# Kernel tuning notes

Hardware: AMD Instinct MI355X
Metric: run time of the kernel (lower is better)

The kernel has to match this reference:

```python
import jax, jax.numpy as jnp
import numpy as np

C, H, W = 3, 224, 224
P = 14  # patches per row
PS = H // P  # 16
PATCH_DIM = C * PS * PS  # 768
HIDDEN = 768


def patchify(images):
    # images: [n, c, h, w] -> [n, P*P, c*PS*PS], flatten order (c, ph, pw)
    n = images.shape[0]
    x = images.reshape(n, C, P, PS, P, PS)
    x = x.transpose(0, 2, 4, 1, 3, 5)  # [n, Pi, Pj, c, ps, ps]
    return x.reshape(n, P * P, PATCH_DIM)


def setup_inputs() -> dict:
    key = jax.random.key(0)
    k1, k2, k3 = jax.random.split(key, 3)
    images = jax.random.normal(k1, (128, C, H, W), dtype=jnp.float32)
    # nn.Linear(patch_embedding_dim, hidden_dim): weight [out, in], bias [out]
    bound = 1.0 / np.sqrt(PATCH_DIM)
    W_lin = jax.random.uniform(k2, (HIDDEN, PATCH_DIM), minval=-bound, maxval=bound, dtype=jnp.float32)
    b_lin = jax.random.uniform(k3, (HIDDEN,), minval=-bound, maxval=bound, dtype=jnp.float32)
    cls_token = jnp.ones((1, HIDDEN), dtype=jnp.float32)
    return {"images": images, "W_lin": W_lin, "b_lin": b_lin, "cls_token": cls_token}


def reference(images, W_lin, b_lin, cls_token):
    patches = patchify(images)                        # [n, 196, 768]
    hidden = jnp.einsum('npd,hd->nph', patches, W_lin) + b_lin  # [n, 196, H]
    n = images.shape[0]
    cls = jnp.broadcast_to(cls_token[None], (n, 1, HIDDEN))
    return jnp.concatenate([cls, hidden], axis=1)     # [n, 197, H]
```

## Files before the change

### kernel.cpp

```cpp
#include <hip/hip_runtime.h>
#include <cstdint>


#define PGRID 14
#define PSZ   16
#define CHN   3
#define IMGW  224
#define KDIM  768
#define NDIM  768
#define NPATCH 196
#define K32   24

typedef short bf16x8 __attribute__((ext_vector_type(8)));
typedef short short8v __attribute__((ext_vector_type(8)));
typedef float f32x4  __attribute__((ext_vector_type(4)));

__device__ __forceinline__ short bf16rne(float f) {
    uint32_t u = __builtin_bit_cast(uint32_t, f);
    u += 0x7FFFu + ((u >> 16) & 1u);
    return (short)(u >> 16);
}

__device__ __forceinline__ short8v cvt8(float4 v0, float4 v1) {
    short8v s;
    s[0] = bf16rne(v0.x); s[1] = bf16rne(v0.y); s[2] = bf16rne(v0.z); s[3] = bf16rne(v0.w);
    s[4] = bf16rne(v1.x); s[5] = bf16rne(v1.y); s[6] = bf16rne(v1.z); s[7] = bf16rne(v1.w);
    return s;
}

__global__ __launch_bounds__(256) void prep_patch(
    const float* __restrict__ img, short* __restrict__ A, int M)
{
    int t = blockIdx.x * 256 + threadIdx.x;
    if (t >= M * 96) return;
    int mlow = t & 15;
    int r    = t >> 4;
    int G    = r / 96;
    int k8   = r - G * 96;
    int m    = G * 16 + mlow;
    int k  = k8 * 8;
    int c  = k >> 8;
    int ph = (k >> 4) & 15;
    int pw = k & 15;
    int im = m / NPATCH;
    int p  = m - im * NPATCH;
    int Pi = p / PGRID;
    int Pj = p - Pi * PGRID;
    const float* src = img + (((long)(im * CHN + c) * IMGW + Pi * PSZ + ph) * IMGW + Pj * PSZ + pw);
    float4 v0 = *(const float4*)src;
    float4 v1 = *(const float4*)(src + 4);
    int k32  = k8 >> 2;
    int quad = k8 & 3;
    int lane = mlow | (quad << 4);
    *(short8v*)(A + (((long)G * K32 + k32) << 9) + lane * 8) = cvt8(v0, v1);
}

__global__ __launch_bounds__(256) void prep_small(
    const float* __restrict__ Wl, const float* __restrict__ cls,
    short* __restrict__ Wb, float* __restrict__ out, int n_img)
{
    int t = blockIdx.x * 256 + threadIdx.x;
    const int WCH = KDIM * NDIM / 8;
    if (t < WCH) {
        int nlow = t & 15;
        int r    = t >> 4;
        int G    = r / 96;
        int k8   = r - G * 96;
        int n    = G * 16 + nlow;
        float4 v0 = *(const float4*)(Wl + (long)n * KDIM + k8 * 8);
        float4 v1 = *(const float4*)(Wl + (long)n * KDIM + k8 * 8 + 4);
        int k32  = k8 >> 2;
        int quad = k8 & 3;
        int lane = nlow | (quad << 4);
        *(short8v*)(Wb + (((long)G * K32 + k32) << 9) + lane * 8) = cvt8(v0, v1);
    } else {
        int u = t - WCH;
        if (u < n_img * 96) {
            int im = u / 96;
            int k8 = u - im * 96;
            float4 v0 = *(const float4*)(cls + k8 * 8);
            float4 v1 = *(const float4*)(cls + k8 * 8 + 4);
            float* dst = out + (long)im * 197 * NDIM + k8 * 8;
            *(float4*)dst = v0;
            *(float4*)(dst + 4) = v1;
        }
    }
}

__global__ __launch_bounds__(256, 3) void vit_gemm5(
    const short* __restrict__ A, const short* __restrict__ B,
    const float* __restrict__ bias, float* __restrict__ out,
    int M, int mgroups)
{
    const int bid = blockIdx.x;
    const int xcd = bid & 7;
    const int s   = bid >> 3;
    const int gq  = s / 6;
    const int j   = s - gq * 6;
    const int g   = gq * 8 + xcd;
    if (g >= mgroups) return;
    const int m0 = g * 128;
    const int n0 = j * 128;

    const int tid  = threadIdx.x;
    const int wave = tid >> 6;
    const int lane = tid & 63;
    const int wq   = lane >> 4;
    const int lr   = lane & 15;
    const int wm   = (wave & 1) * 64;
    const int wn   = (wave >> 1) * 64;

    const short* Ab = A + (((long)((m0 + wm) >> 4) * K32) << 9) + lane * 8;
    const short* Bb = B + (((long)((n0 + wn) >> 4) * K32) << 9) + lane * 8;
    const long fstride = (long)K32 << 9;

    f32x4 acc[4][4] = {};
    bf16x8 a0[4], b0[4], a1[4], b1[4];

#define LD(da, db, kk) { _Pragma("unroll") for (int i = 0; i < 4; ++i) { \
        da[i] = *(const bf16x8*)(Ab + i * fstride + ((kk) << 9)); \
        db[i] = *(const bf16x8*)(Bb + i * fstride + ((kk) << 9)); } }
#define MM(aa, bb) { _Pragma("unroll") for (int i = 0; i < 4; ++i) \
        _Pragma("unroll") for (int q = 0; q < 4; ++q) \
        acc[i][q] = __builtin_amdgcn_mfma_f32_16x16x32_bf16(aa[i], bb[q], acc[i][q], 0, 0, 0); }

    LD(a0, b0, 0);
    for (int k = 0; k < K32; k += 2) {
        LD(a1, b1, k + 1);
        MM(a0, b0);
        if (k + 2 < K32) LD(a0, b0, k + 2);
        MM(a1, b1);
    }
#undef LD
#undef MM

    float bv[4];
    #pragma unroll
    for (int q = 0; q < 4; ++q) bv[q] = bias[n0 + wn + q * 16 + lr];

    const int mw = m0 + wm;
    #pragma unroll
    for (int i = 0; i < 4; ++i) {
        #pragma unroll
        for (int r = 0; r < 4; ++r) {
            int gm = mw + i * 16 + wq * 4 + r;
            if (gm < M) {
                int im = gm / NPATCH;
                int p  = gm - im * NPATCH;
                float* orow = out + ((long)im * 197 + 1 + p) * NDIM + n0 + wn + lr;
                #pragma unroll
                for (int q = 0; q < 4; ++q)
                    orow[q * 16] = acc[i][q][r] + bv[q];
            }
        }
    }
}

#define LDSTR 40
__global__ __launch_bounds__(256) void vit_gemm_fb(
    const float* __restrict__ img, const float* __restrict__ Wl,
    const float* __restrict__ bias, float* __restrict__ out, int n_img)
{
    const int M = n_img * NPATCH;
    __shared__ short As[128 * LDSTR];
    __shared__ short Bs[128 * LDSTR];
    const int tid = threadIdx.x;
    const int m0 = blockIdx.y * 128;
    const int n0 = blockIdx.x * 128;
    const int col4  = tid & 7;
    const int rbase = tid >> 3;
    long arow[4];
    for (int rr = 0; rr < 4; ++rr) {
        int m = m0 + rbase + rr * 32;
        int mm = (m < M) ? m : (M - 1);
        int im = mm / NPATCH;
        int p  = mm % NPATCH;
        int Pi = p / PGRID;
        int Pj = p % PGRID;
        arow[rr] = ((long)(im * CHN) * IMGW + Pi * PSZ) * IMGW + Pj * PSZ;
    }
    const int lane = tid & 63;
    const int wave = tid >> 6;
    const int wm = (wave & 1) * 64;
    const int wn = (wave >> 1) * 64;
    const int wq = lane >> 4;
    const int lr = lane & 15;
    f32x4 acc[4][4] = {};
    for (int k0 = 0; k0 < KDIM; k0 += 32) {
        {
            int k  = k0 + col4 * 4;
            int c  = k >> 8;
            int ph = (k >> 4) & 15;
            int pw = k & 15;
            long koff = (long)(c * IMGW + ph) * IMGW + pw;
            #pragma unroll
            for (int rr = 0; rr < 4; ++rr) {
                const float4 v = *(const float4*)(img + arow[rr] + koff);
                int row = rbase + rr * 32;
                short4 s;
                s.x = bf16rne(v.x); s.y = bf16rne(v.y);
                s.z = bf16rne(v.z); s.w = bf16rne(v.w);
                *(short4*)(&As[row * LDSTR + col4 * 4]) = s;
            }
        }
        {
            int k = k0 + col4 * 4;
            #pragma unroll
            for (int rr = 0; rr < 4; ++rr) {
                int nrow = rbase + rr * 32;
                const float4 v = *(const float4*)(Wl + (long)(n0 + nrow) * KDIM + k);
                short4 s;
                s.x = bf16rne(v.x); s.y = bf16rne(v.y);
                s.z = bf16rne(v.z); s.w = bf16rne(v.w);
                *(short4*)(&Bs[nrow * LDSTR + col4 * 4]) = s;
            }
        }
        __syncthreads();
        bf16x8 a[4], b[4];
        #pragma unroll
        for (int i = 0; i < 4; ++i)
            a[i] = *(const bf16x8*)(&As[(wm + i * 16 + lr) * LDSTR + wq * 8]);
        #pragma unroll
        for (int i = 0; i < 4; ++i)
            b[i] = *(const bf16x8*)(&Bs[(wn + i * 16 + lr) * LDSTR + wq * 8]);
        #pragma unroll
        for (int i = 0; i < 4; ++i)
            #pragma unroll
            for (int j = 0; j < 4; ++j)
                acc[i][j] = __builtin_amdgcn_mfma_f32_16x16x32_bf16(a[i], b[j], acc[i][j], 0, 0, 0);
        __syncthreads();
    }
    float bv[4];
    #pragma unroll
    for (int j = 0; j < 4; ++j) bv[j] = bias[n0 + wn + j * 16 + lr];
    #pragma unroll
    for (int i = 0; i < 4; ++i) {
        #pragma unroll
        for (int r = 0; r < 4; ++r) {
            int gm = m0 + wm + i * 16 + wq * 4 + r;
            if (gm < M) {
                int im = gm / NPATCH;
                int p  = gm % NPATCH;
                long orow = ((long)im * 197 + 1 + p) * (long)NDIM;
                #pragma unroll
                for (int j = 0; j < 4; ++j)
                    out[orow + n0 + wn + j * 16 + lr] = acc[i][j][r] + bv[j];
            }
        }
    }
}

__global__ __launch_bounds__(256) void cls_fill(
    const float* __restrict__ cls, float* __restrict__ out, int n_img)
{
    int i = blockIdx.x * 256 + threadIdx.x;
    if (i < n_img * NDIM) {
        int im = i / NDIM;
        int n  = i - im * NDIM;
        out[(long)im * 197 * NDIM + n] = cls[n];
    }
}

extern "C" void kernel_launch(void* const* d_in, const int* in_sizes, int n_in,
                              void* d_out, int out_size, void* d_ws, size_t ws_size,
                              hipStream_t stream) {
    const float* img  = (const float*)d_in[0];
    const float* Wl   = (const float*)d_in[1];
    const float* bias = (const float*)d_in[2];
    const float* cls  = (const float*)d_in[3];
    float* out = (float*)d_out;

    int n_img = in_sizes[0] / (CHN * IMGW * IMGW);
    int M = n_img * NPATCH;
    int mgroups = (M + 127) / 128;
    long Mpad = (long)mgroups * 128;

    size_t need = (size_t)(Mpad * KDIM + (long)KDIM * NDIM) * sizeof(short);
    if (ws_size >= need) {
        short* A_ws = (short*)d_ws;
        short* Wb   = A_ws + Mpad * KDIM;

        prep_patch<<<(M * 96 + 255) / 256, 256, 0, stream>>>(img, A_ws, M);
        int small_total = KDIM * NDIM / 8 + n_img * 96;
        prep_small<<<(small_total + 255) / 256, 256, 0, stream>>>(Wl, cls, Wb, out, n_img);

        int gpad = (mgroups + 7) & ~7;
        int nblocks = gpad * 6;
        vit_gemm5<<<nblocks, 256, 0, stream>>>(A_ws, Wb, bias, out, M, mgroups);
    } else {
        int mb = (M + 127) / 128;
        dim3 grid(NDIM / 128, mb);
        vit_gemm_fb<<<grid, 256, 0, stream>>>(img, Wl, bias, out, n_img);
        int cls_elems = n_img * NDIM;
        cls_fill<<<(cls_elems + 255) / 256, 256, 0, stream>>>(cls, out, n_img);
    }
}
```

Before: 193.3 us.

## Switch GEMM to 32x32x16 MFMA with 256x128 tiles and matching pre-swizzle

Replaces the 16x16x32 bf16 MFMA with 32x32x16 MFMA and changes the prepacked A/B layouts to 32-row fragments. The block tile grows from 128x128 to 256x128, with each wave owning a 64x128 strip. That cuts A-fragment reloads per MFMA and the number of B reloads across blocks. In exchange it uses more accumulator registers (occupancy hint dropped from 3 to 2), gives fewer blocks (300 instead of 600), and the output stores are scattered in a different pattern.

```diff
diff --git a/kernel.cpp b/kernel.cpp
--- a/kernel.cpp
+++ b/kernel.cpp
@@ -9,11 +9,12 @@
 #define KDIM  768
 #define NDIM  768
 #define NPATCH 196
-#define K32   24
+#define K16   48
+#define FSTR  24576
 
 typedef short bf16x8 __attribute__((ext_vector_type(8)));
 typedef short short8v __attribute__((ext_vector_type(8)));
-typedef float f32x4  __attribute__((ext_vector_type(4)));
+typedef float f32x16 __attribute__((ext_vector_type(16)));
 
 __device__ __forceinline__ short bf16rne(float f) {
     uint32_t u = __builtin_bit_cast(uint32_t, f);
@@ -33,11 +34,11 @@
 {
     int t = blockIdx.x * 256 + threadIdx.x;
     if (t >= M * 96) return;
-    int mlow = t & 15;
-    int r    = t >> 4;
+    int mlow = t & 31;
+    int r    = t >> 5;
     int G    = r / 96;
     int k8   = r - G * 96;
-    int m    = G * 16 + mlow;
+    int m    = G * 32 + mlow;
     int k  = k8 * 8;
     int c  = k >> 8;
     int ph = (k >> 4) & 15;
@@ -49,10 +50,9 @@
     const float* src = img + (((long)(im * CHN + c) * IMGW + Pi * PSZ + ph) * IMGW + Pj * PSZ + pw);
     float4 v0 = *(const float4*)src;
     float4 v1 = *(const float4*)(src + 4);
-    int k32  = k8 >> 2;
-    int quad = k8 & 3;
-    int lane = mlow | (quad << 4);
-    *(short8v*)(A + (((long)G * K32 + k32) << 9) + lane * 8) = cvt8(v0, v1);
+    int chunk = k8 >> 1;
+    int lane  = mlow | ((k8 & 1) << 5);
+    *(short8v*)(A + (((long)G * K16 + chunk) << 9) + lane * 8) = cvt8(v0, v1);
 }
 
 __global__ __launch_bounds__(256) void prep_small(
@@ -62,17 +62,16 @@
     int t = blockIdx.x * 256 + threadIdx.x;
     const int WCH = KDIM * NDIM / 8;
     if (t < WCH) {
-        int nlow = t & 15;
-        int r    = t >> 4;
+        int nlow = t & 31;
+        int r    = t >> 5;
         int G    = r / 96;
         int k8   = r - G * 96;
-        int n    = G * 16 + nlow;
+        int n    = G * 32 + nlow;
         float4 v0 = *(const float4*)(Wl + (long)n * KDIM + k8 * 8);
         float4 v1 = *(const float4*)(Wl + (long)n * KDIM + k8 * 8 + 4);
-        int k32  = k8 >> 2;
-        int quad = k8 & 3;
-        int lane = nlow | (quad << 4);
-        *(short8v*)(Wb + (((long)G * K32 + k32) << 9) + lane * 8) = cvt8(v0, v1);
+        int chunk = k8 >> 1;
+        int lane  = nlow | ((k8 & 1) << 5);
+        *(short8v*)(Wb + (((long)G * K16 + chunk) << 9) + lane * 8) = cvt8(v0, v1);
     } else {
         int u = t - WCH;
         if (u < n_img * 96) {
@@ -87,7 +86,7 @@
     }
 }
 
-__global__ __launch_bounds__(256, 3) void vit_gemm5(
+__global__ __launch_bounds__(256, 2) void vit_gemm6(
     const short* __restrict__ A, const short* __restrict__ B,
     const float* __restrict__ bias, float* __restrict__ out,
     int M, int mgroups)
@@ -99,58 +98,59 @@
     const int j   = s - gq * 6;
     const int g   = gq * 8 + xcd;
     if (g >= mgroups) return;
-    const int m0 = g * 128;
+    const int m0 = g * 256;
     const int n0 = j * 128;
 
     const int tid  = threadIdx.x;
     const int wave = tid >> 6;
     const int lane = tid & 63;
-    const int wq   = lane >> 4;
-    const int lr   = lane & 15;
-    const int wm   = (wave & 1) * 64;
-    const int wn   = (wave >> 1) * 64;
-
-    const short* Ab = A + (((long)((m0 + wm) >> 4) * K32) << 9) + lane * 8;
-    const short* Bb = B + (((long)((n0 + wn) >> 4) * K32) << 9) + lane * 8;
-    const long fstride = (long)K32 << 9;
-
-    f32x4 acc[4][4] = {};
-    bf16x8 a0[4], b0[4], a1[4], b1[4];
-
-#define LD(da, db, kk) { _Pragma("unroll") for (int i = 0; i < 4; ++i) { \
-        da[i] = *(const bf16x8*)(Ab + i * fstride + ((kk) << 9)); \
-        db[i] = *(const bf16x8*)(Bb + i * fstride + ((kk) << 9)); } }
-#define MM(aa, bb) { _Pragma("unroll") for (int i = 0; i < 4; ++i) \
+    const int wm   = wave * 64;
+
+    const short* Ab = A + (((long)((m0 + wm) >> 5) * K16) << 9) + lane * 8;
+    const short* Bb = B + (((long)(n0 >> 5) * K16) << 9) + lane * 8;
+
+    f32x16 acc[2][4] = {};
+    bf16x8 a0[2], b0[4], a1[2], b1[4];
+
+#define LD(da, db, cc) { \
+        _Pragma("unroll") for (int i = 0; i < 2; ++i) \
+            da[i] = *(const bf16x8*)(Ab + i * FSTR + ((cc) << 9)); \
         _Pragma("unroll") for (int q = 0; q < 4; ++q) \
-        acc[i][q] = __builtin_amdgcn_mfma_f32_16x16x32_bf16(aa[i], bb[q], acc[i][q], 0, 0, 0); }
+            db[q] = *(const bf16x8*)(Bb + q * FSTR + ((cc) << 9)); }
+#define MM(aa, bb) { _Pragma("unroll") for (int i = 0; i < 2; ++i) \
+        _Pragma("unroll") for (int q = 0; q < 4; ++q) \
+        acc[i][q] = __builtin_amdgcn_mfma_f32_32x32x16_bf16(aa[i], bb[q], acc[i][q], 0, 0, 0); }
 
     LD(a0, b0, 0);
-    for (int k = 0; k < K32; k += 2) {
-        LD(a1, b1, k + 1);
+    for (int c = 0; c < K16; c += 2) {
+        LD(a1, b1, c + 1);
         MM(a0, b0);
-        if (k + 2 < K32) LD(a0, b0, k + 2);
+        if (c + 2 < K16) LD(a0, b0, c + 2);
         MM(a1, b1);
     }
 #undef LD
 #undef MM
 
+    const int col   = lane & 31;
+    const int rhalf = (lane >> 5) * 4;
+
     float bv[4];
     #pragma unroll
-    for (int q = 0; q < 4; ++q) bv[q] = bias[n0 + wn + q * 16 + lr];
-
-    const int mw = m0 + wm;
-    #pragma unroll
-    for (int i = 0; i < 4; ++i) {
-        #pragma unroll
-        for (int r = 0; r < 4; ++r) {
-            int gm = mw + i * 16 + wq * 4 + r;
+    for (int q = 0; q < 4; ++q) bv[q] = bias[n0 + q * 32 + col];
+
+    #pragma unroll
+    for (int i = 0; i < 2; ++i) {
+        #pragma unroll
+        for (int r = 0; r < 16; ++r) {
+            int row = (r & 3) + 8 * (r >> 2) + rhalf;
+            int gm  = m0 + wm + i * 32 + row;
             if (gm < M) {
                 int im = gm / NPATCH;
                 int p  = gm - im * NPATCH;
-                float* orow = out + ((long)im * 197 + 1 + p) * NDIM + n0 + wn + lr;
+                float* orow = out + ((long)im * 197 + 1 + p) * NDIM + n0 + col;
                 #pragma unroll
                 for (int q = 0; q < 4; ++q)
-                    orow[q * 16] = acc[i][q][r] + bv[q];
+                    orow[q * 32] = acc[i][q][r] + bv[q];
             }
         }
     }
@@ -185,6 +185,7 @@
     const int wn = (wave >> 1) * 64;
     const int wq = lane >> 4;
     const int lr = lane & 15;
+    typedef float f32x4 __attribute__((ext_vector_type(4)));
     f32x4 acc[4][4] = {};
     for (int k0 = 0; k0 < KDIM; k0 += 32) {
         {
@@ -272,8 +273,8 @@
 
     int n_img = in_sizes[0] / (CHN * IMGW * IMGW);
     int M = n_img * NPATCH;
-    int mgroups = (M + 127) / 128;
-    long Mpad = (long)mgroups * 128;
+    int mgroups = (M + 255) / 256;
+    long Mpad = (long)mgroups * 256;
 
     size_t need = (size_t)(Mpad * KDIM + (long)KDIM * NDIM) * sizeof(short);
     if (ws_size >= need) {
@@ -286,7 +287,7 @@
 
         int gpad = (mgroups + 7) & ~7;
         int nblocks = gpad * 6;
-        vit_gemm5<<<nblocks, 256, 0, stream>>>(A_ws, Wb, bias, out, M, mgroups);
+        vit_gemm6<<<nblocks, 256, 0, stream>>>(A_ws, Wb, bias, out, M, mgroups);
     } else {
         int mb = (M + 127) / 128;
         dim3 grid(NDIM / 128, mb);
```

Measured after the change: 195.4 us. Within noise of the previous version (+1.1%).
